# Performance work log

Measured on AMD Instinct MI355X. Metric: run time of the kernel, lower is better.

## Reference

```python
import jax, jax.numpy as jnp
import numpy as np

FEATURE_COUNT = 41024
PAD_IDX = FEATURE_COUNT  # padding_idx in nn.Embedding
HIDDEN = 256
BATCH = 8192
BAG = 32


def setup_inputs() -> dict:
    key = jax.random.key(0)
    ks = jax.random.split(key, 9)
    emb = jax.random.normal(ks[0], (FEATURE_COUNT + 1, HIDDEN), jnp.float32) * 0.05
    emb = emb.at[PAD_IDX].set(0.0)  # padding row is zero, as in nn.Embedding(padding_idx=...)
    us = jax.random.randint(ks[1], (BATCH, BAG), 0, FEATURE_COUNT + 1)
    them = jax.random.randint(ks[2], (BATCH, BAG), 0, FEATURE_COUNT + 1)
    fc1_w = jax.random.normal(ks[3], (32, 2 * HIDDEN), jnp.float32) * 0.04
    fc1_b = jax.random.normal(ks[4], (32,), jnp.float32) * 0.01
    fc2_w = jax.random.normal(ks[5], (32, 32), jnp.float32) * 0.1
    fc2_b = jax.random.normal(ks[6], (32,), jnp.float32) * 0.01
    fc3_w = jax.random.normal(ks[7], (1, 32), jnp.float32) * 0.1
    fc3_b = jax.random.normal(ks[8], (1,), jnp.float32) * 0.01
    return {"us": us, "them": them, "emb": emb,
            "fc1_w": fc1_w, "fc1_b": fc1_b,
            "fc2_w": fc2_w, "fc2_b": fc2_b,
            "fc3_w": fc3_w, "fc3_b": fc3_b}


def _bag_sum(emb, idx):
    # gather [B, BAG, H], zero padded slots, sum over bag -> [B, H]
    e = emb[idx] * (idx != PAD_IDX)[..., None].astype(emb.dtype)
    return e.sum(axis=1)


def reference(us, them, emb, fc1_w, fc1_b, fc2_w, fc2_b, fc3_w, fc3_b):
    acc_us = _bag_sum(emb, us)      # [B, H]
    acc_them = _bag_sum(emb, them)  # [B, H]
    x = jnp.concatenate([acc_us, acc_them], axis=1)  # [B, 2H]
    x = jnp.clip(x @ fc1_w.T + fc1_b, 0.0, 1.0)
    x = jnp.clip(x @ fc2_w.T + fc2_b, 0.0, 1.0)
    return jnp.tanh(x @ fc3_w.T + fc3_b)  # [B, 1]
```

## Files before the change

kernel.cpp:

```cpp
#include <hip/hip_runtime.h>
#include <hip/hip_bf16.h>

constexpr int HIDDEN = 256;
constexpr int BAG    = 32;
constexpr int FEAT   = 41025;
constexpr int NJ     = 64;
constexpr int LDSS   = 264;

using bf16x8 = __attribute__((ext_vector_type(8))) short;
using f32x4  = __attribute__((ext_vector_type(4))) float;

__device__ inline unsigned short f2bf(float f) {
    __hip_bfloat16 h = __float2bfloat16(f);
    return __builtin_bit_cast(unsigned short, h);
}
__device__ inline void cvt_store(unsigned short* dst, float4 v) {
    ushort4 b; b.x = f2bf(v.x); b.y = f2bf(v.y); b.z = f2bf(v.z); b.w = f2bf(v.w);
    *reinterpret_cast<ushort4*>(dst) = b;
}

__global__ __launch_bounds__(256, 2) void k0_project_mfma(
    const float*    __restrict__ emb,
    const float*    __restrict__ fc1_w,
    unsigned short* __restrict__ P)
{
    __shared__ unsigned short a_lds[64 * LDSS];
    __shared__ unsigned short b_lds[64 * LDSS];

    const int tid = threadIdx.x;
    const int f0  = blockIdx.x * 64;
    const float4* emb4 = reinterpret_cast<const float4*>(emb);
    const float4* w4   = reinterpret_cast<const float4*>(fc1_w);

    float4 aR[16], bR[16];
#pragma unroll
    for (int s = 0; s < 16; ++s) {
        const int idx4 = s * 256 + tid;
        const int row  = idx4 >> 6;
        const int kq4  = idx4 & 63;
        int grow = f0 + row; if (grow >= FEAT) grow = FEAT - 1;
        aR[s] = emb4[(size_t)grow * 64 + kq4];
    }
#pragma unroll
    for (int s = 0; s < 16; ++s)
        bR[s] = w4[s * 256 + tid];

#pragma unroll
    for (int s = 0; s < 16; ++s) {
        const int idx4 = s * 256 + tid;
        const int row  = idx4 >> 6;
        const int kq4  = idx4 & 63;
        cvt_store(&a_lds[row * LDSS + kq4 * 4], aR[s]);
    }
#pragma unroll
    for (int s = 0; s < 16; ++s) {
        const int idx4 = s * 256 + tid;
        const int jr  = idx4 >> 7;
        const int kc4 = idx4 & 127;
        const int j   = jr + ((kc4 >= 64) ? 32 : 0);
        const int k4  = kc4 & 63;
        cvt_store(&b_lds[j * LDSS + k4 * 4], bR[s]);
    }
    __syncthreads();

    const int lane = tid & 63, wave = tid >> 6;
    const int g = lane >> 4, ml = lane & 15;
    const int mw = wave * 16;

    f32x4 acc[4] = {{0.f,0.f,0.f,0.f},{0.f,0.f,0.f,0.f},
                    {0.f,0.f,0.f,0.f},{0.f,0.f,0.f,0.f}};
#pragma unroll
    for (int kt = 0; kt < 8; ++kt) {
        const bf16x8 af = *reinterpret_cast<const bf16x8*>(
            &a_lds[(mw + ml) * LDSS + kt * 32 + g * 8]);
#pragma unroll
        for (int nt = 0; nt < 4; ++nt) {
            const bf16x8 bf = *reinterpret_cast<const bf16x8*>(
                &b_lds[(nt * 16 + ml) * LDSS + kt * 32 + g * 8]);
            acc[nt] = __builtin_amdgcn_mfma_f32_16x16x32_bf16(af, bf, acc[nt], 0, 0, 0);
        }
    }

#pragma unroll
    for (int nt = 0; nt < 4; ++nt) {
#pragma unroll
        for (int r = 0; r < 4; ++r) {
            const int f = f0 + mw + g * 4 + r;
            if (f < FEAT)
                P[(size_t)f * NJ + nt * 16 + ml] = f2bf(acc[nt][r]);
        }
    }
}

__global__ __launch_bounds__(256) void k1_gather_mlp(
    const int*            __restrict__ us,
    const int*            __restrict__ them,
    const unsigned short* __restrict__ P,
    const float* __restrict__ b1,
    const float* __restrict__ w2, const float* __restrict__ b2,
    const float* __restrict__ w3, const float* __restrict__ b3,
    float*       __restrict__ out)
{
    __shared__ float w2_lds[32][33];
    __shared__ float y1_lds[8][33];

    const int tid  = threadIdx.x;
    const int wave = tid >> 6;
    const int lane = tid & 63;

    for (int k = tid; k < 32 * 32; k += 256)
        w2_lds[k >> 5][k & 31] = w2[k];

    const int rowA = blockIdx.x * 8 + wave * 2;
    const int rowB = rowA + 1;
    int idxA, idxB;
    {
        const int* upA = us   + (size_t)rowA * BAG;
        const int* tpA = them + (size_t)rowA * BAG;
        idxA = (lane < BAG) ? upA[lane] : tpA[lane - BAG];
        const int* upB = us   + (size_t)rowB * BAG;
        const int* tpB = them + (size_t)rowB * BAG;
        idxB = (lane < BAG) ? upB[lane] : tpB[lane - BAG];
    }

    const int  l4     = lane & 15;
    const bool isB    = lane >= 32;
    const bool isThem = (lane >> 4) & 1;
    const unsigned colbyte = (isThem ? 64u : 0u) + (unsigned)l4 * 4u;
    const char* Pb = (const char*)P;

    float accx = 0.f, accy = 0.f;
#pragma unroll
    for (int i = 0; i < BAG; ++i) {
        const int fuA = __builtin_amdgcn_readlane(idxA, i);
        const int ftA = __builtin_amdgcn_readlane(idxA, BAG + i);
        const int fuB = __builtin_amdgcn_readlane(idxB, i);
        const int ftB = __builtin_amdgcn_readlane(idxB, BAG + i);
        const int fA  = isThem ? ftA : fuA;
        const int fB  = isThem ? ftB : fuB;
        const int f   = isB ? fB : fA;
        const unsigned u = *(const unsigned*)(Pb + (((unsigned)f << 7) + colbyte));
        accx += __builtin_bit_cast(float, u << 16);
        accy += __builtin_bit_cast(float, u & 0xffff0000u);
    }
    accx += __shfl_xor(accx, 16);
    accy += __shfl_xor(accy, 16);

    __syncthreads();

    const int yrow = wave * 2 + (isB ? 1 : 0);
    if (!isThem) {
        const int c0 = l4 * 2;
        y1_lds[yrow][c0]     = fminf(fmaxf(accx + b1[c0],     0.f), 1.f);
        y1_lds[yrow][c0 + 1] = fminf(fmaxf(accy + b1[c0 + 1], 0.f), 1.f);
    }
    __syncthreads();

    const int j = lane & 31;
    float s = b2[j];
#pragma unroll
    for (int k = 0; k < 32; ++k)
        s += y1_lds[yrow][k] * w2_lds[j][k];
    float r3 = fminf(fmaxf(s, 0.f), 1.f) * w3[j];
    r3 += __shfl_xor(r3, 16); r3 += __shfl_xor(r3, 8); r3 += __shfl_xor(r3, 4);
    r3 += __shfl_xor(r3, 2);  r3 += __shfl_xor(r3, 1);
    if (j == 0) out[isB ? rowB : rowA] = tanhf(r3 + b3[0]);
}

__global__ __launch_bounds__(256) void nnue_fused(
    const int*   __restrict__ us,
    const int*   __restrict__ them,
    const float* __restrict__ emb,
    const float* __restrict__ w1, const float* __restrict__ b1,
    const float* __restrict__ w2, const float* __restrict__ b2,
    const float* __restrict__ w3, const float* __restrict__ b3,
    float*       __restrict__ out)
{
    __shared__ float x_lds[4][2 * HIDDEN];
    __shared__ float y1_lds[4][32];
    __shared__ float y2_lds[4][32];

    const int tid  = threadIdx.x;
    const int wave = tid >> 6;
    const int lane = tid & 63;
    const int row  = blockIdx.x * 4 + wave;

    int myidx;
    {
        const int* up = us   + (size_t)row * BAG;
        const int* tp = them + (size_t)row * BAG;
        myidx = (lane < BAG) ? up[lane] : tp[lane - BAG];
    }
    const float4* emb4 = reinterpret_cast<const float4*>(emb);
    float4 accU = make_float4(0.f, 0.f, 0.f, 0.f);
    float4 accT = make_float4(0.f, 0.f, 0.f, 0.f);
#pragma unroll
    for (int i = 0; i < BAG; ++i) {
        const int iu = __shfl(myidx, i);
        const int it = __shfl(myidx, BAG + i);
        const float4 vu = emb4[(size_t)iu * (HIDDEN / 4) + lane];
        const float4 vt = emb4[(size_t)it * (HIDDEN / 4) + lane];
        accU.x += vu.x; accU.y += vu.y; accU.z += vu.z; accU.w += vu.w;
        accT.x += vt.x; accT.y += vt.y; accT.z += vt.z; accT.w += vt.w;
    }
    {
        float4* xv = reinterpret_cast<float4*>(&x_lds[wave][0]);
        xv[lane]      = accU;
        xv[64 + lane] = accT;
    }
    __syncthreads();
    {
        const int r    = tid >> 6;
        const int sub  = tid & 63;
        const int j    = sub >> 1;
        const int half = sub & 1;
        const float4* xr = reinterpret_cast<const float4*>(&x_lds[r][0]) + half * 64;
        const float4* wr = reinterpret_cast<const float4*>(w1 + (size_t)j * (2 * HIDDEN)) + half * 64;
        float s = 0.f;
#pragma unroll 8
        for (int k = 0; k < 64; ++k) {
            const float4 xk = xr[k];
            const float4 wk = wr[k];
            s += xk.x * wk.x + xk.y * wk.y + xk.z * wk.z + xk.w * wk.w;
        }
        s += __shfl_xor(s, 1);
        if (half == 0) { s += b1[j]; y1_lds[r][j] = fminf(fmaxf(s, 0.f), 1.f); }
    }
    __syncthreads();
    if (tid < 4 * 32) {
        const int r = tid >> 5;
        const int j = tid & 31;
        const float* wr = w2 + j * 32;
        float s = b2[j];
#pragma unroll
        for (int k = 0; k < 32; ++k) s += y1_lds[r][k] * wr[k];
        y2_lds[r][j] = fminf(fmaxf(s, 0.f), 1.f);
    }
    __syncthreads();
    if (tid < 4) {
        const int r = tid;
        float s = b3[0];
#pragma unroll
        for (int k = 0; k < 32; ++k) s += y2_lds[r][k] * w3[k];
        out[blockIdx.x * 4 + r] = tanhf(s);
    }
}

extern "C" void kernel_launch(void* const* d_in, const int* in_sizes, int n_in,
                              void* d_out, int out_size, void* d_ws, size_t ws_size,
                              hipStream_t stream) {
    const int*   us   = (const int*)  d_in[0];
    const int*   them = (const int*)  d_in[1];
    const float* emb  = (const float*)d_in[2];
    const float* w1   = (const float*)d_in[3];
    const float* b1   = (const float*)d_in[4];
    const float* w2   = (const float*)d_in[5];
    const float* b2   = (const float*)d_in[6];
    const float* w3   = (const float*)d_in[7];
    const float* b3   = (const float*)d_in[8];
    float* out = (float*)d_out;

    const int batch = in_sizes[0] / BAG;
    const size_t p_bytes = (size_t)FEAT * NJ * sizeof(unsigned short);

    if (ws_size >= p_bytes && batch % 8 == 0) {
        unsigned short* P = (unsigned short*)d_ws;
        const int grid0 = (FEAT + 63) / 64;
        k0_project_mfma<<<grid0, 256, 0, stream>>>(emb, w1, P);
        k1_gather_mlp<<<batch / 8, 256, 0, stream>>>(us, them, P,
                                                     b1, w2, b2, w3, b3, out);
    } else {
        nnue_fused<<<(batch + 3) / 4, 256, 0, stream>>>(us, them, emb,
                                                        w1, b1, w2, b2, w3, b3, out);
    }
}
```

Before: 24.92 us.

## Prepack fc1 weights into MFMA B-fragments and keep them in registers

Adds a small pre-kernel that converts fc1_w into bf16 MFMA B-operand fragments in workspace. The projection kernel then loads those fragments directly into registers, dropping the per-block fp32 weight load, bf16 conversion and B staging in LDS. This halves LDS use and removes the B LDS reads from the MFMA loop. In exchange it adds a kernel launch, holds 32 vector registers of weights per thread, and drops the 2-blocks-per-CU launch bound hint.

```diff
diff --git a/kernel.cpp b/kernel.cpp
--- a/kernel.cpp
+++ b/kernel.cpp
@@ -18,21 +18,41 @@
     ushort4 b; b.x = f2bf(v.x); b.y = f2bf(v.y); b.z = f2bf(v.z); b.w = f2bf(v.w);
     *reinterpret_cast<ushort4*>(dst) = b;
 }
-
-__global__ __launch_bounds__(256, 2) void k0_project_mfma(
+__device__ inline bf16x8 pack8(float4 a, float4 b) {
+    bf16x8 r;
+    r[0]=(short)f2bf(a.x); r[1]=(short)f2bf(a.y); r[2]=(short)f2bf(a.z); r[3]=(short)f2bf(a.w);
+    r[4]=(short)f2bf(b.x); r[5]=(short)f2bf(b.y); r[6]=(short)f2bf(b.z); r[7]=(short)f2bf(b.w);
+    return r;
+}
+
+__global__ __launch_bounds__(256) void k_pre_wfrag(
+    const float* __restrict__ fc1_w,
+    int4*        __restrict__ Wfrag)
+{
+    const int e    = blockIdx.x * 256 + threadIdx.x;
+    const int lane = e & 63, fid = e >> 6;
+    const int nt = fid >> 3, kt = fid & 7;
+    const int g = lane >> 4, ml = lane & 15;
+    const int j = nt * 16 + ml;
+    const float* src = fc1_w + (size_t)(j & 31) * 512 + ((j >> 5) << 8)
+                      + kt * 32 + g * 8;
+    const float4 x0 = *reinterpret_cast<const float4*>(src);
+    const float4 x1 = *reinterpret_cast<const float4*>(src + 4);
+    Wfrag[e] = __builtin_bit_cast(int4, pack8(x0, x1));
+}
+
+__global__ __launch_bounds__(256) void k0_project_mfma(
     const float*    __restrict__ emb,
-    const float*    __restrict__ fc1_w,
+    const int4*     __restrict__ Wfrag,
     unsigned short* __restrict__ P)
 {
     __shared__ unsigned short a_lds[64 * LDSS];
-    __shared__ unsigned short b_lds[64 * LDSS];
 
     const int tid = threadIdx.x;
     const int f0  = blockIdx.x * 64;
     const float4* emb4 = reinterpret_cast<const float4*>(emb);
-    const float4* w4   = reinterpret_cast<const float4*>(fc1_w);
-
-    float4 aR[16], bR[16];
+
+    float4 aR[16];
 #pragma unroll
     for (int s = 0; s < 16; ++s) {
         const int idx4 = s * 256 + tid;
@@ -41,9 +61,13 @@
         int grow = f0 + row; if (grow >= FEAT) grow = FEAT - 1;
         aR[s] = emb4[(size_t)grow * 64 + kq4];
     }
-#pragma unroll
-    for (int s = 0; s < 16; ++s)
-        bR[s] = w4[s * 256 + tid];
+    const int lane = tid & 63, wave = tid >> 6;
+    bf16x8 breg[4][8];
+#pragma unroll
+    for (int nt = 0; nt < 4; ++nt)
+#pragma unroll
+        for (int kt = 0; kt < 8; ++kt)
+            breg[nt][kt] = __builtin_bit_cast(bf16x8, Wfrag[(nt * 8 + kt) * 64 + lane]);
 
 #pragma unroll
     for (int s = 0; s < 16; ++s) {
@@ -52,18 +76,8 @@
         const int kq4  = idx4 & 63;
         cvt_store(&a_lds[row * LDSS + kq4 * 4], aR[s]);
     }
-#pragma unroll
-    for (int s = 0; s < 16; ++s) {
-        const int idx4 = s * 256 + tid;
-        const int jr  = idx4 >> 7;
-        const int kc4 = idx4 & 127;
-        const int j   = jr + ((kc4 >= 64) ? 32 : 0);
-        const int k4  = kc4 & 63;
-        cvt_store(&b_lds[j * LDSS + k4 * 4], bR[s]);
-    }
-    __syncthreads();
-
-    const int lane = tid & 63, wave = tid >> 6;
+    __syncthreads();
+
     const int g = lane >> 4, ml = lane & 15;
     const int mw = wave * 16;
 
@@ -74,11 +88,9 @@
         const bf16x8 af = *reinterpret_cast<const bf16x8*>(
             &a_lds[(mw + ml) * LDSS + kt * 32 + g * 8]);
 #pragma unroll
-        for (int nt = 0; nt < 4; ++nt) {
-            const bf16x8 bf = *reinterpret_cast<const bf16x8*>(
-                &b_lds[(nt * 16 + ml) * LDSS + kt * 32 + g * 8]);
-            acc[nt] = __builtin_amdgcn_mfma_f32_16x16x32_bf16(af, bf, acc[nt], 0, 0, 0);
-        }
+        for (int nt = 0; nt < 4; ++nt)
+            acc[nt] = __builtin_amdgcn_mfma_f32_16x16x32_bf16(af, breg[nt][kt],
+                                                              acc[nt], 0, 0, 0);
     }
 
 #pragma unroll
@@ -261,12 +273,15 @@
     float* out = (float*)d_out;
 
     const int batch = in_sizes[0] / BAG;
-    const size_t p_bytes = (size_t)FEAT * NJ * sizeof(unsigned short);
-
-    if (ws_size >= p_bytes && batch % 8 == 0) {
+    const size_t p_bytes  = (size_t)FEAT * NJ * sizeof(unsigned short);
+    const size_t wf_bytes = 2048 * sizeof(int4);
+
+    if (ws_size >= p_bytes + wf_bytes && batch % 8 == 0) {
         unsigned short* P = (unsigned short*)d_ws;
+        int4* Wfrag = (int4*)((char*)d_ws + p_bytes);
         const int grid0 = (FEAT + 63) / 64;
-        k0_project_mfma<<<grid0, 256, 0, stream>>>(emb, w1, P);
+        k_pre_wfrag<<<8, 256, 0, stream>>>(w1, Wfrag);
+        k0_project_mfma<<<grid0, 256, 0, stream>>>(emb, Wfrag, P);
         k1_gather_mlp<<<batch / 8, 256, 0, stream>>>(us, them, P,
                                                      b1, w2, b2, w3, b3, out);
     } else {
```

Result: slower. 29.13 us (+16.9%).
